# Performance work log

Hardware: AMD Instinct MI355X
Metric: run time of the kernel (lower is better)

The kernel has to match this reference:

```python
import jax, jax.numpy as jnp
import numpy as np
from jax.scipy.special import logsumexp

NEG = -1e9  # matches INF=1e9 in the original (finite -INF)
B, M, L = 64, 16, 128


def _parallel_backward_mask(Lq, Mq):
    # Faithful port of CachedTensorMixin.parallel_backward_mask (static, numpy).
    mm = np.zeros((Lq, Lq, Lq), np.float32)
    em = np.zeros((Lq, Lq, Lq), np.float32)
    triu = np.triu(np.ones((Lq, Lq), np.float32))
    for j in range(Lq):
        i = Lq - 1 - j
        mm[j, :Lq - i, i:Lq] = triu[:Lq - i, :Lq - i]
        em[j, :Lq - i, i:Lq] = triu[:Lq - i, :Lq - i]
        mm[j, 0, :i] = 1.0
    return jnp.asarray(mm[:, :Mq]), jnp.asarray(em[:, :Mq])


def _forward_algorithm(t, mask, lengths):
    # t, mask: [B, M, L]; semi-Markov forward log-sum-exp DP as a scan over end positions.
    Bq, Mq, Lq = t.shape
    base = t + (1.0 - mask) * NEG  # masked edges: t - INF (matches fill(-INF); [bmask]=0; +=t)

    def step(w, xs):
        # w[:, m] = log_alpha[node j - m]
        base_j, mask_j = xs  # [B, M] column for end position j
        cand = base_j + mask_j * w  # node->edge: log_alpha added only where mask==1
        la_next = logsumexp(cand, axis=-1)  # log_alpha[j+1]
        w_new = jnp.concatenate([la_next[:, None], w[:, :-1]], axis=1)
        return w_new, (la_next, cand)

    w0 = jnp.zeros((Bq, Mq), t.dtype)  # log_alpha[0] = 0
    _, (las, cands) = jax.lax.scan(step, w0, (base.transpose(2, 0, 1), mask.transpose(2, 0, 1)))
    la_all = jnp.concatenate([jnp.zeros((1, Bq), t.dtype), las], axis=0)  # [L+1, B]
    log_alpha = la_all[lengths, jnp.arange(Bq)]
    edge_log_alphas = cands.transpose(1, 2, 0)  # [B, M, L]
    return log_alpha, edge_log_alphas


def _entropy(t, mask, lengths):
    # Entropy semiring: H[j+1] = sum_e q_e * (H[src(e)] - log q_e), q_e = edge posterior.
    Bq, Mq, Lq = t.shape
    base = t + (1.0 - mask) * NEG

    def step(carry, xs):
        w_la, w_h = carry
        base_j, mask_j = xs
        cand = base_j + mask_j * w_la
        la_next = logsumexp(cand, axis=-1)
        valid = mask_j > 0
        q = jnp.where(valid, jnp.exp(cand - la_next[:, None]), 0.0)
        contrib = jnp.where(valid, q * (w_h + la_next[:, None] - cand), 0.0)
        h_next = contrib.sum(-1)
        w_la_new = jnp.concatenate([la_next[:, None], w_la[:, :-1]], axis=1)
        w_h_new = jnp.concatenate([h_next[:, None], w_h[:, :-1]], axis=1)
        return (w_la_new, w_h_new), (h_next, contrib)

    w0 = jnp.zeros((Bq, Mq), t.dtype)
    _, (hs, contribs) = jax.lax.scan(step, (w0, w0), (base.transpose(2, 0, 1), mask.transpose(2, 0, 1)))
    h_all = jnp.concatenate([jnp.zeros((1, Bq), t.dtype), hs], axis=0)
    ent = h_all[lengths, jnp.arange(Bq)]
    edge_ent = contribs.transpose(1, 2, 0)  # [B, M, L]
    return ent, edge_ent


def reference(fwd_ts, fwd_ms, bwd_ts, bwd_ms, lengths, override_M):
    Bq, Mq, Lq = fwd_ts.shape
    Muse = min(Mq, Lq, int(override_M))  # == Mq (16) for these specs
    log_alpha, edge_log_alpha = _forward_algorithm(fwd_ts, fwd_ms, lengths)
    ent, edge_ent = _entropy(fwd_ts, fwd_ms, lengths)
    mmask, emask = _parallel_backward_mask(Lq, Muse)  # [L, M, L]
    bwd_t2 = (bwd_ts[:, None] * emask[None]).reshape(Bq * Lq, Muse, Lq)
    bwd_m2 = (bwd_ms[:, None] * mmask[None]).reshape(Bq * Lq, Muse, Lq)
    bwd_lengths = jnp.repeat(lengths, Lq)
    log_betas, elb = _forward_algorithm(bwd_t2, bwd_m2, bwd_lengths)
    log_betas = log_betas.reshape(Bq, Lq)
    elb = elb.reshape(Bq, Lq, Muse, Lq)
    elb = elb * emask + NEG * (1.0 - emask)
    return (fwd_ts, fwd_ms, log_alpha, edge_log_alpha, log_betas, elb, ent, edge_ent)


def setup_inputs() -> dict:
    key = jax.random.key(0)
    k1, k2 = jax.random.split(key)
    lengths = jax.random.randint(k1, (B,), L // 2, L + 1).astype(jnp.int32)
    m_idx = jnp.arange(M)[None, :, None]
    j_idx = jnp.arange(L)[None, None, :]
    len_b = lengths[:, None, None]
    # edge [m, j] (length m+1 ending at char j) valid iff m <= j < len  (full-vocab lattice)
    fwd_ms = ((m_idx <= j_idx) & (j_idx < len_b)).astype(jnp.float32)
    bwd_ms = fwd_ms
    fwd_ts = jax.random.normal(k2, (B, M, L), jnp.float32) - 2.0  # log-space unit weights
    # backward encoding is the left-right flip: bwd[m, len-1-s] == fwd[m, s+m]
    src = jnp.clip(len_b - 1 - j_idx + m_idx, 0, L - 1)
    src = jnp.broadcast_to(src, (B, M, L))
    bwd_ts = jnp.take_along_axis(fwd_ts, src, axis=2)
    return {"fwd_ts": fwd_ts, "fwd_ms": fwd_ms, "bwd_ts": bwd_ts, "bwd_ms": bwd_ms,
            "lengths": lengths, "override_M": M}
```

## Files before the change

kernel.cpp:

```cpp
#include <hip/hip_runtime.h>

#define NEGC  (-1000000000.0f)
#define NEG2C (-1.4426950408889634e9f)
#define LOG2E 1.4426950408889634f
#define LN2   0.6931471805599453f

constexpr int B_=64, M_=16, L_=128;
constexpr long OFF_FTS=0;
constexpr long OFF_FMS=OFF_FTS+(long)B_*M_*L_;
constexpr long OFF_LA =OFF_FMS+(long)B_*M_*L_;
constexpr long OFF_ELA=OFF_LA+B_;
constexpr long OFF_LB =OFF_ELA+(long)B_*M_*L_;
constexpr long OFF_ELB=OFF_LB+(long)B_*L_;
constexpr long OFF_ENT=OFF_ELB+(long)B_*L_*M_*L_;
constexpr long OFF_EE =OFF_ENT+B_;

constexpr int LDSS=132;
constexpr int RSTR=33;
constexpr int GSTR=536;
constexpr int ET_OFF=2112;
constexpr int TL_OFF=4224;
constexpr int WV_T=2144;
constexpr int FR=17, FT=280, FG=560;

template<int CTRL>
__device__ __forceinline__ float dppf(float x){
  return __int_as_float(__builtin_amdgcn_update_dpp(0,__float_as_int(x),CTRL,0xF,0xF,true));
}
__device__ __forceinline__ float red16(float x){
  x += dppf<0xB1>(x); x += dppf<0x4E>(x); x += dppf<0x141>(x); x += dppf<0x140>(x);
  return x;
}
__device__ __forceinline__ float red8(float x){
  x += dppf<0xB1>(x); x += dppf<0x4E>(x); x += dppf<0x141>(x);
  return x;
}
__device__ __forceinline__ float fexp2(float x){
#if __has_builtin(__builtin_amdgcn_exp2f)
  return __builtin_amdgcn_exp2f(x);
#else
  return __builtin_exp2f(x);
#endif
}
__device__ __forceinline__ float flog2(float x){
#if __has_builtin(__builtin_amdgcn_logf)
  return __builtin_amdgcn_logf(x);
#else
  return __builtin_log2f(x);
#endif
}
__device__ __forceinline__ float frcp(float x){
#if __has_builtin(__builtin_amdgcn_rcpf)
  return __builtin_amdgcn_rcpf(x);
#else
  return 1.0f/x;
#endif
}

__global__ __launch_bounds__(128) void tok_main(
    const float* __restrict__ fwd_ts, const float* __restrict__ fwd_ms,
    const float* __restrict__ bwd_ts, const float* __restrict__ bwd_ms,
    const int* __restrict__ lengths, float* __restrict__ out)
{
  __shared__ float smem[8960];
  const int tid  = threadIdx.x;
  const int blk  = blockIdx.x;
  const int lane = tid & 63;
  const int wv   = tid >> 6;
  const int m    = lane & 15;
  const int g    = lane >> 4;

  if (blk >= 4) {
    const int bk  = blk - 4;
    const int b   = bk >> 4;
    const int sub = bk & 15;
    const int j   = sub + 16*(wv*4 + g);

    if (tid < 16) {
      const float4* s0 = (const float4*)fwd_ts;
      const float4* s1 = (const float4*)fwd_ms;
      int idx = bk*16 + tid;
      float4 v = (idx < 8192) ? s0[idx] : s1[idx - 8192];
      ((float4*)out)[idx] = v;
    }

    const float4* gts = (const float4*)(bwd_ts + (long)b*2048);
    #pragma unroll
    for (int it=0; it<4; ++it){
      int t4 = it*128 + tid;
      float4 a = gts[t4];
      int mr = t4 >> 5, l4 = (t4 & 31) << 2;
      float* dt = smem + mr*LDSS + l4;
      float* de = smem + ET_OFF + mr*LDSS + l4;
      float x0=a.x*LOG2E, x1=a.y*LOG2E, x2=a.z*LOG2E, x3=a.w*LOG2E;
      dt[0]=x0; dt[1]=x1; dt[2]=x2; dt[3]=x3;
      de[0]=fexp2(x0); de[1]=fexp2(x1); de[2]=fexp2(x2); de[3]=fexp2(x3);
    }
    __syncthreads();

    const int len = lengths[b];
    const int lenm1 = len - 1;
    const int i0 = 127 - j;
    const int thr  = i0 + m;
    const int thrp = (m==0) ? 0 : thr;
    float W = 1.0f, ref2 = 0.0f, la2k = 0.0f, totl = 1.0f;
    const float* rowt = smem + m*LDSS;
    const float* rowe = smem + ET_OFF + m*LDSS;
    float* wbase = smem + TL_OFF + wv*WV_T;
    float* buf = wbase + g*GSTR + m*RSTR;
    const int fm = lane >> 3;
    const int fk = (lane & 7) << 2;

    for (int l0 = 0; l0 < 128; l0 += 4){
      float4 t4v = *(const float4*)(rowt + l0);
      float4 e4v = *(const float4*)(rowe + l0);
      float ta[4]={t4v.x,t4v.y,t4v.z,t4v.w};
      float ea[4]={e4v.x,e4v.y,e4v.z,e4v.w};
      #pragma unroll
      for (int kk=0; kk<4; ++kk){
        const int l = l0 + kk;
        const bool em = (l >= thr);
        const bool uw = (l >= thrp) && (l < len);
        float e  = em ? ea[kk] : 1.0f;
        float x  = W * e;
        float s  = uw ? x : 0.0f;
        float tot = red16(s);
        float w2 = ref2 + flog2(fmaxf(W, 1e-38f));
        float c2 = (em ? ta[kk] : 0.0f) + (uw ? w2 : NEG2C);
        buf[l & 31] = em ? c2*LN2 : NEGC;
        if (l == lenm1) la2k = ref2 + flog2(tot);
        float sh = dppf<0x111>(W);
        W = (m==0) ? tot : sh;
        totl = tot;
      }
      if ((l0 & 15) == 12){
        float ef = __builtin_floorf(flog2(fmaxf(totl, 1e-30f)));
        W *= fexp2(-ef);
        ref2 += ef;
      }
      if ((l0 & 31) == 28){
        const int lb = l0 - 28;
        #pragma unroll
        for (int g2=0; g2<4; ++g2){
          const int j2 = sub + 16*(wv*4 + g2);
          float* db = out + OFF_ELB + ((long)(b*128 + j2) << 11) + lb;
          const float* s1p = wbase + g2*GSTR + fm*RSTR + fk;
          *(float4*)(db + fm*128 + fk) =
              make_float4(s1p[0], s1p[1], s1p[2], s1p[3]);
          const float* s2p = wbase + g2*GSTR + (fm+8)*RSTR + fk;
          *(float4*)(db + (fm+8)*128 + fk) =
              make_float4(s2p[0], s2p[1], s2p[2], s2p[3]);
        }
      }
    }
    if (m == 0) out[OFF_LB + (long)b*128 + j] = la2k * LN2;

  } else {
    const int p  = lane & 7;
    const int gw = lane >> 3;
    const int b = blk*16 + wv*8 + gw;
    const int len = lengths[b];
    const int lenm1 = len - 1;
    const float* ftA = fwd_ts + ((long)b*16 + p)*128;
    const float* ftB = fwd_ts + ((long)b*16 + p + 8)*128;
    float w2A=0.f, w2B=0.f, whA=0.f, whB=0.f, stab=0.f, la_keep=0.f, h_keep=0.f;
    float* base = smem + (wv*8 + gw)*FG;
    float* eA  = base + p*FR;
    float* eB  = base + (p+8)*FR;
    float* hA  = base + FT + p*FR;
    float* hB  = base + FT + (p+8)*FR;
    const int fm2 = lane >> 2;
    const int fk2 = (lane & 3) << 2;

    float4 a4 = *(const float4*)(ftA);
    float4 b4 = *(const float4*)(ftB);
    for (int j0 = 0; j0 < 128; j0 += 4){
      float4 a4n, b4n;
      if (j0 < 124){ a4n = *(const float4*)(ftA + j0 + 4);
                     b4n = *(const float4*)(ftB + j0 + 4); }
      float tA[4]={a4.x,a4.y,a4.z,a4.w}, tB[4]={b4.x,b4.y,b4.z,b4.w};
      #pragma unroll
      for (int kk=0; kk<4; ++kk){
        const int jj = j0 + kk;
        const bool vA = (p <= jj) && (jj < len);
        const bool vB = (p+8 <= jj) && (jj < len);
        float cA = tA[kk]*LOG2E + (vA ? w2A : NEG2C);
        float cB = tB[kk]*LOG2E + (vB ? w2B : NEG2C);
        float dA = cA - stab, dB = cB - stab;
        float sA = fexp2(dA), sB = fexp2(dB);
        float tot = red8(sA + sB);
        float lg = flog2(tot);
        float la = stab + lg;
        float rt = frcp(tot);
        float coA = vA ? (sA*rt) * (whA + (lg - dA)*LN2) : 0.f;
        float coB = vB ? (sB*rt) * (whB + (lg - dB)*LN2) : 0.f;
        float h = red8(coA + coB);
        eA[jj & 15] = cA*LN2;
        eB[jj & 15] = cB*LN2;
        hA[jj & 15] = coA;
        hB[jj & 15] = coB;
        if (jj == lenm1){ la_keep = la; h_keep = h; }
        float mirW = dppf<0x141>(w2A);
        float mirH = dppf<0x141>(whA);
        float sWA = dppf<0x111>(w2A), sWB = dppf<0x111>(w2B);
        float sHA = dppf<0x111>(whA), sHB = dppf<0x111>(whB);
        w2A = (p==0) ? la   : sWA;
        w2B = (p==0) ? mirW : sWB;
        whA = (p==0) ? h    : sHA;
        whB = (p==0) ? mirH : sHB;
        stab = la;
      }
      if ((j0 & 15) == 12){
        const int jb = j0 - 12;
        #pragma unroll
        for (int g2=0; g2<8; ++g2){
          const int b2 = blk*16 + wv*8 + g2;
          const float* sb = smem + (wv*8 + g2)*FG;
          const float* sp = sb + fm2*FR + fk2;
          *(float4*)(out + OFF_ELA + ((long)b2*16 + fm2)*128 + jb + fk2) =
              make_float4(sp[0], sp[1], sp[2], sp[3]);
          const float* sp2 = sb + FT + fm2*FR + fk2;
          *(float4*)(out + OFF_EE + ((long)b2*16 + fm2)*128 + jb + fk2) =
              make_float4(sp2[0], sp2[1], sp2[2], sp2[3]);
        }
      }
      a4 = a4n; b4 = b4n;
    }
    if (p == 0){
      out[OFF_LA + b] = la_keep * LN2;
      out[OFF_ENT + b] = h_keep;
    }
  }
}

extern "C" void kernel_launch(void* const* d_in, const int* in_sizes, int n_in,
                              void* d_out, int out_size, void* d_ws, size_t ws_size,
                              hipStream_t stream) {
  const float* fts = (const float*)d_in[0];
  const float* fms = (const float*)d_in[1];
  const float* bts = (const float*)d_in[2];
  const float* bms = (const float*)d_in[3];
  const int*   len = (const int*)d_in[4];
  float* out = (float*)d_out;
  hipLaunchKernelGGL(tok_main, dim3(1028), dim3(128), 0, stream,
                     fts, fms, bts, bms, len, out);
}
```

Baseline: 108.1 us.

## Split backward DP into serial recurrence and deferred log/emit phases per 32-chunk

Restructures the backward-edge loop into 32-step chunks. The serial phase now runs only the multiply, DPP reduction and shift, and records W values in registers. The log2, candidate computation and LDS writes are moved into a separate non-serial phase, taking transcendental work off the dependency chain. Renormalisation now uses integer exponent extraction with ldexp instead of floor(log2), and exp values are prefetched into register arrays per chunk. The cost is much higher register pressure (several 32-float arrays) and a possible small change in rounding.

```diff
diff --git a/kernel.cpp b/kernel.cpp
--- a/kernel.cpp
+++ b/kernel.cpp
@@ -92,18 +92,16 @@
       int mr = t4 >> 5, l4 = (t4 & 31) << 2;
       float* dt = smem + mr*LDSS + l4;
       float* de = smem + ET_OFF + mr*LDSS + l4;
-      float x0=a.x*LOG2E, x1=a.y*LOG2E, x2=a.z*LOG2E, x3=a.w*LOG2E;
-      dt[0]=x0; dt[1]=x1; dt[2]=x2; dt[3]=x3;
-      de[0]=fexp2(x0); de[1]=fexp2(x1); de[2]=fexp2(x2); de[3]=fexp2(x3);
+      dt[0]=a.x; dt[1]=a.y; dt[2]=a.z; dt[3]=a.w;
+      de[0]=fexp2(a.x*LOG2E); de[1]=fexp2(a.y*LOG2E);
+      de[2]=fexp2(a.z*LOG2E); de[3]=fexp2(a.w*LOG2E);
     }
     __syncthreads();
 
     const int len = lengths[b];
     const int lenm1 = len - 1;
-    const int i0 = 127 - j;
-    const int thr  = i0 + m;
+    const int thr  = 127 - j + m;
     const int thrp = (m==0) ? 0 : thr;
-    float W = 1.0f, ref2 = 0.0f, la2k = 0.0f, totl = 1.0f;
     const float* rowt = smem + m*LDSS;
     const float* rowe = smem + ET_OFF + m*LDSS;
     float* wbase = smem + TL_OFF + wv*WV_T;
@@ -111,49 +109,97 @@
     const int fm = lane >> 3;
     const int fk = (lane & 7) << 2;
 
-    for (int l0 = 0; l0 < 128; l0 += 4){
-      float4 t4v = *(const float4*)(rowt + l0);
-      float4 e4v = *(const float4*)(rowe + l0);
-      float ta[4]={t4v.x,t4v.y,t4v.z,t4v.w};
-      float ea[4]={e4v.x,e4v.y,e4v.z,e4v.w};
-      #pragma unroll
-      for (int kk=0; kk<4; ++kk){
-        const int l = l0 + kk;
-        const bool em = (l >= thr);
-        const bool uw = (l >= thrp) && (l < len);
-        float e  = em ? ea[kk] : 1.0f;
-        float x  = W * e;
-        float s  = uw ? x : 0.0f;
+    float W = 1.0f, keepT = 1.0f;
+    int refI = 0, keepR = 0;
+
+    float Ev[32];
+    {
+      const float4* ep = (const float4*)rowe;
+      #pragma unroll
+      for (int r=0; r<8; ++r){
+        float4 v = ep[r];
+        Ev[4*r]=v.x; Ev[4*r+1]=v.y; Ev[4*r+2]=v.z; Ev[4*r+3]=v.w;
+      }
+    }
+
+    for (int c=0; c<4; ++c){
+      const int lb = c << 5;
+      const int thrC  = thr  - lb;
+      const int thrpC = thrp - lb;
+      const int lenC  = len  - lb;
+      const int lm1C  = lenm1 - lb;
+      const int refEntry = refI;
+      int refMid = refI;
+      float Wh[32];
+
+      #pragma unroll
+      for (int t=0; t<32; ++t){
+        const bool em = (t >= thrC);
+        const bool uw = (t >= thrpC) && (t < lenC);
+        float e = em ? Ev[t] : 1.0f;
+        float x = W * e;
+        float s = uw ? x : 0.0f;
         float tot = red16(s);
-        float w2 = ref2 + flog2(fmaxf(W, 1e-38f));
-        float c2 = (em ? ta[kk] : 0.0f) + (uw ? w2 : NEG2C);
-        buf[l & 31] = em ? c2*LN2 : NEGC;
-        if (l == lenm1) la2k = ref2 + flog2(tot);
+        keepT = (t == lm1C) ? tot : keepT;
+        keepR = (t == lm1C) ? refI : keepR;
+        Wh[t] = W;
         float sh = dppf<0x111>(W);
         W = (m==0) ? tot : sh;
-        totl = tot;
-      }
-      if ((l0 & 15) == 12){
-        float ef = __builtin_floorf(flog2(fmaxf(totl, 1e-30f)));
-        W *= fexp2(-ef);
-        ref2 += ef;
-      }
-      if ((l0 & 31) == 28){
-        const int lb = l0 - 28;
+        if (t==15 || t==31){
+          int ef = (int)((__float_as_uint(tot) >> 23) & 255) - 127;
+          W = ldexpf(W, -ef);
+          refI += ef;
+          if (t==15) refMid = refI;
+        }
+      }
+
+      float Tn[32], Evn[32];
+      {
+        const float4* tp = (const float4*)(rowt + lb);
         #pragma unroll
-        for (int g2=0; g2<4; ++g2){
-          const int j2 = sub + 16*(wv*4 + g2);
-          float* db = out + OFF_ELB + ((long)(b*128 + j2) << 11) + lb;
-          const float* s1p = wbase + g2*GSTR + fm*RSTR + fk;
-          *(float4*)(db + fm*128 + fk) =
-              make_float4(s1p[0], s1p[1], s1p[2], s1p[3]);
-          const float* s2p = wbase + g2*GSTR + (fm+8)*RSTR + fk;
-          *(float4*)(db + (fm+8)*128 + fk) =
-              make_float4(s2p[0], s2p[1], s2p[2], s2p[3]);
-        }
-      }
-    }
-    if (m == 0) out[OFF_LB + (long)b*128 + j] = la2k * LN2;
+        for (int r=0; r<8; ++r){
+          float4 v = tp[r];
+          Tn[4*r]=v.x; Tn[4*r+1]=v.y; Tn[4*r+2]=v.z; Tn[4*r+3]=v.w;
+        }
+        if (c < 3){
+          const float4* ep = (const float4*)(rowe + lb + 32);
+          #pragma unroll
+          for (int r=0; r<8; ++r){
+            float4 v = ep[r];
+            Evn[4*r]=v.x; Evn[4*r+1]=v.y; Evn[4*r+2]=v.z; Evn[4*r+3]=v.w;
+          }
+        }
+      }
+
+      const float refF0 = (float)refEntry, refF1 = (float)refMid;
+      #pragma unroll
+      for (int t=0; t<32; ++t){
+        const bool em = (t >= thrC);
+        const bool uw = (t >= thrpC) && (t < lenC);
+        float lg = flog2(fmaxf(Wh[t], 1e-30f));
+        float wn = (lg + (t < 16 ? refF0 : refF1)) * LN2;
+        float cc = (em ? Tn[t] : 0.0f) + (uw ? wn : NEGC);
+        buf[t] = em ? cc : NEGC;
+      }
+
+      #pragma unroll
+      for (int g2=0; g2<4; ++g2){
+        const int j2 = sub + 16*(wv*4 + g2);
+        float* db = out + OFF_ELB + ((long)(b*128 + j2) << 11) + lb;
+        const float* s1p = wbase + g2*GSTR + fm*RSTR + fk;
+        *(float4*)(db + fm*128 + fk) = make_float4(s1p[0], s1p[1], s1p[2], s1p[3]);
+        const float* s2p = wbase + g2*GSTR + (fm+8)*RSTR + fk;
+        *(float4*)(db + (fm+8)*128 + fk) = make_float4(s2p[0], s2p[1], s2p[2], s2p[3]);
+      }
+
+      if (c < 3){
+        #pragma unroll
+        for (int t=0; t<32; ++t) Ev[t] = Evn[t];
+      }
+    }
+    if (m == 0)
+      out[OFF_LB + (long)b*128 + j] =
+          (flog2(fmaxf(keepT, 1e-30f)) + (float)keepR) * LN2;
 
   } else {
     const int p  = lane & 7;
```

Result: no change. 108.9 us (+0.7%).
